# Kernel optimization log

Measured on AMD Instinct MI355X. Metric: run time of the kernel, lower is better.

## Reference

```python
import jax, jax.numpy as jnp
import numpy as np

B, T, V, D = 8, 256, 32, 256


def setup_inputs() -> dict:
    key = jax.random.key(0)
    k1, k2 = jax.random.split(key)
    # scale by 0.1 so exp(q.k) stays well within fp32 range (dot std ~ 0.1^2*sqrt(D))
    feature = jax.random.normal(k1, (B, T, V, D), dtype=jnp.float32) * 0.1
    feature_aug = jax.random.normal(k2, (B, T, V, D), dtype=jnp.float32) * 0.1
    return {"feature": feature, "feature_aug": feature_aug}


def reference(feature, feature_aug):
    # match torch permute(0,2,1,3): [B,T,V,D] -> [B,V,T,D]
    f = jnp.transpose(feature, (0, 2, 1, 3))      # [B,V,Tq,D]
    fa = jnp.transpose(feature_aug, (0, 2, 1, 3))  # [B,V,Tk,D]
    # all-pairs QK^T scores: [B_i, B_j, V, Tq, Tk]
    scores = jnp.einsum('ivqd,jvkd->ijvqk', f, fa)
    E = jnp.exp(scores)
    # positive (j == i): ap = exp(scores[i,i]).sum over V, Tq -> [B, Tk]
    diag = jnp.einsum('iivqk->ivqk', E)           # [B,V,Tq,Tk]
    ap_exp = diag.sum(axis=(1, 2))                # [B, Tk]
    # negatives (j != i): sum over j,V,Tk minus the j==i part -> [B, Tq]
    total = E.sum(axis=(1, 2, 4))                 # [B, Tq]
    self_part = diag.sum(axis=(1, 3))             # [B, Tq]
    an_exp = total - self_part                    # [B, Tq]
    # per-anchor loss vector [T]; original sums over anchors then takes .mean()
    loss_vec = -jnp.log(ap_exp / an_exp)          # [B, T]
    return loss_vec.sum(axis=0).mean()
```

## Files before the change

kernel.cpp:

```cpp
#include <hip/hip_runtime.h>
#include <hip/hip_bf16.h>


typedef __attribute__((ext_vector_type(4))) float f32x4;
typedef __attribute__((ext_vector_type(4))) int   i32x4;
typedef __attribute__((ext_vector_type(8))) int   i32x8;
typedef __attribute__((ext_vector_type(8))) __bf16 bf16x8;

#if __has_builtin(__builtin_amdgcn_exp2f)
#define EXP2(x) __builtin_amdgcn_exp2f(x)
#else
#define EXP2(x) exp2f(x)
#endif

__device__ __forceinline__ unsigned short f2bf(float f) {
    unsigned u = __builtin_bit_cast(unsigned, f);
    u += 0x7FFFu + ((u >> 16) & 1u);
    return (unsigned short)(u >> 16);
}

template <bool HI>
__device__ __forceinline__ unsigned cvt2fp8(float a, float b, unsigned old) {
    return __builtin_amdgcn_cvt_pk_fp8_f32(a, b, old, HI);
}
__device__ __forceinline__ unsigned pack4fp8(float x, float y, float z, float w) {
    return cvt2fp8<true>(z, w, cvt2fp8<false>(x, y, 0u));
}

__device__ __forceinline__ void async16(const void* g, void* l) {
    __builtin_amdgcn_global_load_lds(
        (const __attribute__((address_space(1))) unsigned int*)g,
        (__attribute__((address_space(3))) unsigned int*)l,
        16, 0, 0);
}

__device__ __forceinline__ i32x8 cat8(i32x4 lo, i32x4 hi) {
    i32x8 r;
    r[0] = lo[0]; r[1] = lo[1]; r[2] = lo[2]; r[3] = lo[3];
    r[4] = hi[0]; r[5] = hi[1]; r[6] = hi[2]; r[7] = hi[3];
    return r;
}

template <int CTRL>
__device__ __forceinline__ float dpp_add(float x) {
    int y = __builtin_amdgcn_update_dpp(0, __builtin_bit_cast(int, x),
                                        CTRL, 0xf, 0xf, true);
    return x + __builtin_bit_cast(float, y);
}
__device__ __forceinline__ float rowsum16(float x) {
    x = dpp_add<0x111>(x);
    x = dpp_add<0x112>(x);
    x = dpp_add<0x114>(x);
    x = dpp_add<0x118>(x);
    return x;
}

__global__ __launch_bounds__(256) void infonce_repack_fp8(
    const float* __restrict__ feat, const float* __restrict__ feat_aug,
    unsigned char* __restrict__ pA, unsigned char* __restrict__ pB,
    float* __restrict__ counters)
{
    const int row = blockIdx.x;
    const int tid = threadIdx.x;
    if (blockIdx.x == 0 && blockIdx.y == 0) {
        #pragma unroll
        for (int k = 0; k < 24; ++k) counters[k * 256 + tid] = 0.f;
    }
    const bool isA = (blockIdx.y == 0);
    const float sc = isA ? 1.4426950408889634f : 1.0f;
    const float* src = (isA ? feat : feat_aug) + (size_t)row * 8192;
    unsigned char* dst = (isA ? pA : pB) + (size_t)row * 8192;
    #pragma unroll
    for (int it = 0; it < 2; ++it) {
        const int base = it * 4096 + tid * 16;
        const float4 f0 = *(const float4*)(src + base);
        const float4 f1 = *(const float4*)(src + base + 4);
        const float4 f2 = *(const float4*)(src + base + 8);
        const float4 f3 = *(const float4*)(src + base + 12);
        uint4 p;
        p.x = pack4fp8(f0.x*sc, f0.y*sc, f0.z*sc, f0.w*sc);
        p.y = pack4fp8(f1.x*sc, f1.y*sc, f1.z*sc, f1.w*sc);
        p.z = pack4fp8(f2.x*sc, f2.y*sc, f2.z*sc, f2.w*sc);
        p.w = pack4fp8(f3.x*sc, f3.y*sc, f3.z*sc, f3.w*sc);
        *(uint4*)(dst + base) = p;
    }
}

__global__ __launch_bounds__(256, 2) void infonce_main_nl(
    const unsigned char* __restrict__ pA, const unsigned char* __restrict__ pB,
    float* __restrict__ total, float* __restrict__ selfp, float* __restrict__ ap)
{
    __shared__ __align__(16) unsigned char As[128 * 256];
    __shared__ __align__(16) unsigned char Bs[2][64 * 256];
    float (*ls_row2)[128]  = (float (*)[128])(void*)As;
    float (*ls_self2)[128] = (float (*)[128])(void*)(As + 1024);

    const int tid  = threadIdx.x;
    const int lane = tid & 63;
    const int w    = tid >> 6;
    const int wm   = w >> 1;
    const int wn   = w & 1;
    const int lrow = lane & 15;
    const int quad = lane >> 4;

    const int tileM = blockIdx.x;
    const int v     = blockIdx.y;
    const int nD0   = (tileM >> 1) * 4;

    const size_t vOff = (size_t)v * 256;

    {
        const size_t rowM = (size_t)(tileM * 128 + w * 32 + quad) * 8192 + vOff;
        #pragma unroll
        for (int i = 0; i < 8; ++i) {
            const int lg = (lrow ^ ((i * 4 + quad) & 15)) << 4;
            async16(pA + rowM + (size_t)i * 4 * 8192 + lg, &As[(w * 32 + i * 4) * 256]);
        }
    }
    const size_t rowNbase = (size_t)(w * 16 + quad) * 8192 + vOff;
    #pragma unroll
    for (int i = 0; i < 4; ++i) {
        const int lg = (lrow ^ ((i * 4 + quad) & 15)) << 4;
        async16(pB + rowNbase + (size_t)i * 4 * 8192 + lg,
                &Bs[0][(w * 16 + i * 4) * 256]);
    }
    __syncthreads();

    i32x8 af[2][4];
    #pragma unroll
    for (int h = 0; h < 2; ++h)
        #pragma unroll
        for (int t = 0; t < 4; ++t) {
            const int rA = (wm * 64 + t * 16 + lrow) * 256;
            const int g0 = ((h * 8 + quad * 2) ^ lrow) * 16;
            af[h][t] = cat8(*(const i32x4*)&As[rA + g0],
                            *(const i32x4*)&As[rA + (g0 ^ 16)]);
        }

    float rowp[4][4];
    float selfr[4][4];
    #pragma unroll
    for (int t = 0; t < 4; ++t)
        #pragma unroll
        for (int r = 0; r < 4; ++r) { rowp[t][r] = 0.f; selfr[t][r] = 0.f; }

    for (int n = 0; n < 32; ++n) {
        const int b = n & 1;
        if (n < 31) {
            const unsigned char* src = pB + rowNbase + (size_t)(n + 1) * 64 * 8192;
            #pragma unroll
            for (int i = 0; i < 4; ++i) {
                const int lg = (lrow ^ ((i * 4 + quad) & 15)) << 4;
                async16(src + (size_t)i * 4 * 8192 + lg,
                        &Bs[b ^ 1][(w * 16 + i * 4) * 256]);
            }
        }
        f32x4 acc[4][2];
        #pragma unroll
        for (int t = 0; t < 4; ++t)
            #pragma unroll
            for (int tj = 0; tj < 2; ++tj)
                acc[t][tj] = (f32x4){0.f, 0.f, 0.f, 0.f};
        #pragma unroll
        for (int h = 0; h < 2; ++h) {
            i32x8 bf[2];
            #pragma unroll
            for (int tj = 0; tj < 2; ++tj) {
                const int rB = (wn * 32 + tj * 16 + lrow) * 256;
                const int g0 = ((h * 8 + quad * 2) ^ lrow) * 16;
                bf[tj] = cat8(*(const i32x4*)&Bs[b][rB + g0],
                              *(const i32x4*)&Bs[b][rB + (g0 ^ 16)]);
            }
            #pragma unroll
            for (int ti = 0; ti < 4; ++ti)
                #pragma unroll
                for (int tj = 0; tj < 2; ++tj)
                    acc[ti][tj] = __builtin_amdgcn_mfma_scale_f32_16x16x128_f8f6f4(
                        af[h][ti], bf[tj], acc[ti][tj],
                        0, 0, 0, 127, 0, 127);
        }
        const bool diagIter = (n >= nD0) && (n < nD0 + 4);
        float colp0 = 0.f, colp1 = 0.f;
        #pragma unroll
        for (int t = 0; t < 4; ++t)
            #pragma unroll
            for (int r = 0; r < 4; ++r) {
                float e0 = EXP2(acc[t][0][r]);
                float e1 = EXP2(acc[t][1][r]);
                rowp[t][r] += e0 + e1;
                if (diagIter) { selfr[t][r] += e0 + e1; colp0 += e0; colp1 += e1; }
            }
        if (diagIter) {
            float q0 = colp0, q1 = colp1;
            q0 += __shfl_xor(q0, 16); q0 += __shfl_xor(q0, 32);
            q1 += __shfl_xor(q1, 16); q1 += __shfl_xor(q1, 32);
            if (lane < 16) {
                atomicAdd(&ap[n * 64 + wn * 32 + lane], q0);
                atomicAdd(&ap[n * 64 + wn * 32 + 16 + lane], q1);
            }
        }
        __syncthreads();
    }

    #pragma unroll
    for (int t = 0; t < 4; ++t)
        #pragma unroll
        for (int r = 0; r < 4; ++r) {
            float rs = rowsum16(rowp[t][r]);
            float ss = rowsum16(selfr[t][r]);
            if (lrow == 15) {
                const int idx = wm * 64 + t * 16 + quad * 4 + r;
                ls_row2[wn][idx]  = rs;
                ls_self2[wn][idx] = ss;
            }
        }
    __syncthreads();
    if (tid < 128) {
        atomicAdd(&total[tileM * 128 + tid], ls_row2[0][tid] + ls_row2[1][tid]);
    } else {
        const int t2 = tid - 128;
        atomicAdd(&selfp[tileM * 128 + t2], ls_self2[0][t2] + ls_self2[1][t2]);
    }
}

__global__ __launch_bounds__(256) void infonce_main_slow(
    const float* __restrict__ feat, const float* __restrict__ feat_aug,
    float* __restrict__ total, float* __restrict__ selfp, float* __restrict__ ap)
{
    __shared__ __align__(16) unsigned short As[128][72];
    __shared__ __align__(16) unsigned short Bs[128][72];
    __shared__ float ls_row[128];
    __shared__ float ls_col[128];

    const int tid  = threadIdx.x;
    const int lane = tid & 63;
    const int w    = tid >> 6;
    const int wm   = w >> 1;
    const int wn   = w & 1;
    const int lrow = lane & 15;
    const int quad = lane >> 4;

    const int tileM = blockIdx.x & 15;
    const int tileN = blockIdx.x >> 4;
    const int v     = blockIdx.y;
    const bool diag = (tileM >> 1) == (tileN >> 1);

    if (tid < 128) ls_row[tid] = 0.0f;
    else           ls_col[tid - 128] = 0.0f;

    const float* aBase = feat     + (size_t)v * 256;
    const float* bBase = feat_aug + (size_t)v * 256;

    f32x4 acc[4][4];
    #pragma unroll
    for (int i = 0; i < 4; ++i)
        #pragma unroll
        for (int j = 0; j < 4; ++j)
            acc[i][j] = (f32x4){0.f, 0.f, 0.f, 0.f};

    const int srow = tid >> 4;
    const int scol = (tid & 15) * 4;

    for (int s = 0; s < 4; ++s) {
        const int k0 = s * 64;
        if (s) __syncthreads();
        #pragma unroll
        for (int it = 0; it < 8; ++it) {
            const int row = it * 16 + srow;
            const float4 a4 = *(const float4*)(aBase + (size_t)(tileM * 128 + row) * 8192 + k0 + scol);
            const float4 b4 = *(const float4*)(bBase + (size_t)(tileN * 128 + row) * 8192 + k0 + scol);
            uint2 wa, wb;
            wa.x = (unsigned)f2bf(a4.x) | ((unsigned)f2bf(a4.y) << 16);
            wa.y = (unsigned)f2bf(a4.z) | ((unsigned)f2bf(a4.w) << 16);
            wb.x = (unsigned)f2bf(b4.x) | ((unsigned)f2bf(b4.y) << 16);
            wb.y = (unsigned)f2bf(b4.z) | ((unsigned)f2bf(b4.w) << 16);
            *(uint2*)&As[row][scol] = wa;
            *(uint2*)&Bs[row][scol] = wb;
        }
        __syncthreads();
        #pragma unroll
        for (int kk = 0; kk < 64; kk += 32) {
            bf16x8 af[4], bfr[4];
            #pragma unroll
            for (int t = 0; t < 4; ++t) {
                af[t]  = *(const bf16x8*)&As[wm * 64 + t * 16 + lrow][kk + quad * 8];
                bfr[t] = *(const bf16x8*)&Bs[wn * 64 + t * 16 + lrow][kk + quad * 8];
            }
            #pragma unroll
            for (int ti = 0; ti < 4; ++ti)
                #pragma unroll
                for (int tj = 0; tj < 4; ++tj)
                    acc[ti][tj] = __builtin_amdgcn_mfma_f32_16x16x32_bf16(
                        af[ti], bfr[tj], acc[ti][tj], 0, 0, 0);
        }
    }

    float colp[4] = {0.f, 0.f, 0.f, 0.f};
    #pragma unroll
    for (int ti = 0; ti < 4; ++ti) {
        #pragma unroll
        for (int r = 0; r < 4; ++r) {
            float e0 = __expf(acc[ti][0][r]);
            float e1 = __expf(acc[ti][1][r]);
            float e2 = __expf(acc[ti][2][r]);
            float e3 = __expf(acc[ti][3][r]);
            colp[0] += e0; colp[1] += e1; colp[2] += e2; colp[3] += e3;
            float rp = (e0 + e1) + (e2 + e3);
            rp += __shfl_xor(rp, 1);
            rp += __shfl_xor(rp, 2);
            rp += __shfl_xor(rp, 4);
            rp += __shfl_xor(rp, 8);
            if (lrow == 0)
                atomicAdd(&ls_row[wm * 64 + ti * 16 + quad * 4 + r], rp);
        }
    }
    if (diag) {
        #pragma unroll
        for (int tj = 0; tj < 4; ++tj) {
            float q = colp[tj];
            q += __shfl_xor(q, 16);
            q += __shfl_xor(q, 32);
            if (lane < 16)
                atomicAdd(&ls_col[wn * 64 + tj * 16 + lane], q);
        }
    }
    __syncthreads();
    if (tid < 128) {
        const float rs = ls_row[tid];
        const int rowg = tileM * 128 + tid;
        atomicAdd(&total[rowg], rs);
        if (diag) atomicAdd(&selfp[rowg], rs);
    } else if (diag) {
        const int t2 = tid - 128;
        atomicAdd(&ap[tileN * 128 + t2], ls_col[t2]);
    }
}

__global__ __launch_bounds__(256) void infonce_finalize(
    const float* __restrict__ total, const float* __restrict__ selfp,
    const float* __restrict__ ap, float* __restrict__ out)
{
    __shared__ float red[4];
    const int tid = threadIdx.x;
    float s = 0.f;
    for (int e = tid; e < 2048; e += 256) {
        const float an = total[e] - selfp[e];
        s += logf(an / ap[e]);
    }
    #pragma unroll
    for (int m = 32; m >= 1; m >>= 1) s += __shfl_xor(s, m);
    if ((tid & 63) == 0) red[tid >> 6] = s;
    __syncthreads();
    if (tid == 0) out[0] = (red[0] + red[1] + red[2] + red[3]) * (1.0f / 256.0f);
}

extern "C" void kernel_launch(void* const* d_in, const int* in_sizes, int n_in,
                              void* d_out, int out_size, void* d_ws, size_t ws_size,
                              hipStream_t stream) {
    const float* feat     = (const float*)d_in[0];
    const float* feat_aug = (const float*)d_in[1];
    float* total = (float*)d_ws;
    float* selfp = total + 2048;
    float* ap    = selfp + 2048;

    const size_t packBytes = (size_t)2048 * 8192;
    const size_t need = 32768 + 2 * packBytes;
    if (ws_size >= need) {
        unsigned char* pA = (unsigned char*)d_ws + 32768;
        unsigned char* pB = pA + packBytes;
        infonce_repack_fp8<<<dim3(2048, 2), 256, 0, stream>>>(feat, feat_aug, pA, pB, total);
        infonce_main_nl<<<dim3(16, 32), 256, 0, stream>>>(pA, pB, total, selfp, ap);
    } else {
        (void)hipMemsetAsync(d_ws, 0, 3 * 2048 * sizeof(float), stream);
        infonce_main_slow<<<dim3(256, 32), 256, 0, stream>>>(feat, feat_aug, total, selfp, ap);
    }
    infonce_finalize<<<1, 256, 0, stream>>>(total, selfp, ap, (float*)d_out);
}
```

Before: 192.8 us.

## Fuse A-side fp8 packing into main kernel and split N loop across two blocks

Drops the separate fp8 repack of the query features. The main kernel now loads fp32 rows directly into registers and converts them to fp8 with the log2e scale applied, which removes a global write and re-read of the packed A buffer and frees the A shared-memory tile. The N loop over key tiles is split across a new grid z dimension of 2 so there are twice as many blocks, and the occupancy hint is raised to 3. In exchange, each half re-reads the fp32 A rows, and there are more atomic adds into the row totals, with the self term added only by the block that covers the diagonal.

```diff
diff --git a/kernel.cpp b/kernel.cpp
--- a/kernel.cpp
+++ b/kernel.cpp
@@ -12,6 +12,8 @@
 #else
 #define EXP2(x) exp2f(x)
 #endif
+
+#define LOG2E 1.4426950408889634f
 
 __device__ __forceinline__ unsigned short f2bf(float f) {
     unsigned u = __builtin_bit_cast(unsigned, f);
@@ -56,20 +58,17 @@
 }
 
 __global__ __launch_bounds__(256) void infonce_repack_fp8(
-    const float* __restrict__ feat, const float* __restrict__ feat_aug,
-    unsigned char* __restrict__ pA, unsigned char* __restrict__ pB,
+    const float* __restrict__ feat_aug, unsigned char* __restrict__ pB,
     float* __restrict__ counters)
 {
     const int row = blockIdx.x;
     const int tid = threadIdx.x;
-    if (blockIdx.x == 0 && blockIdx.y == 0) {
+    if (row == 0) {
         #pragma unroll
         for (int k = 0; k < 24; ++k) counters[k * 256 + tid] = 0.f;
     }
-    const bool isA = (blockIdx.y == 0);
-    const float sc = isA ? 1.4426950408889634f : 1.0f;
-    const float* src = (isA ? feat : feat_aug) + (size_t)row * 8192;
-    unsigned char* dst = (isA ? pA : pB) + (size_t)row * 8192;
+    const float* src = feat_aug + (size_t)row * 8192;
+    unsigned char* dst = pB + (size_t)row * 8192;
     #pragma unroll
     for (int it = 0; it < 2; ++it) {
         const int base = it * 4096 + tid * 16;
@@ -78,22 +77,21 @@
         const float4 f2 = *(const float4*)(src + base + 8);
         const float4 f3 = *(const float4*)(src + base + 12);
         uint4 p;
-        p.x = pack4fp8(f0.x*sc, f0.y*sc, f0.z*sc, f0.w*sc);
-        p.y = pack4fp8(f1.x*sc, f1.y*sc, f1.z*sc, f1.w*sc);
-        p.z = pack4fp8(f2.x*sc, f2.y*sc, f2.z*sc, f2.w*sc);
-        p.w = pack4fp8(f3.x*sc, f3.y*sc, f3.z*sc, f3.w*sc);
+        p.x = pack4fp8(f0.x, f0.y, f0.z, f0.w);
+        p.y = pack4fp8(f1.x, f1.y, f1.z, f1.w);
+        p.z = pack4fp8(f2.x, f2.y, f2.z, f2.w);
+        p.w = pack4fp8(f3.x, f3.y, f3.z, f3.w);
         *(uint4*)(dst + base) = p;
     }
 }
 
-__global__ __launch_bounds__(256, 2) void infonce_main_nl(
-    const unsigned char* __restrict__ pA, const unsigned char* __restrict__ pB,
+__global__ __launch_bounds__(256, 3) void infonce_main_nl(
+    const float* __restrict__ feat, const unsigned char* __restrict__ pB,
     float* __restrict__ total, float* __restrict__ selfp, float* __restrict__ ap)
 {
-    __shared__ __align__(16) unsigned char As[128 * 256];
     __shared__ __align__(16) unsigned char Bs[2][64 * 256];
-    float (*ls_row2)[128]  = (float (*)[128])(void*)As;
-    float (*ls_self2)[128] = (float (*)[128])(void*)(As + 1024);
+    float (*ls_row2)[128]  = (float (*)[128])(void*)&Bs[0][0];
+    float (*ls_self2)[128] = (float (*)[128])(void*)&Bs[0][1024];
 
     const int tid  = threadIdx.x;
     const int lane = tid & 63;
@@ -105,37 +103,43 @@
 
     const int tileM = blockIdx.x;
     const int v     = blockIdx.y;
+    const int zh    = blockIdx.z;
+    const int n0    = zh * 16;
+    const int n1    = n0 + 16;
     const int nD0   = (tileM >> 1) * 4;
+    const bool hasDiag = (nD0 >= n0) && (nD0 < n1);
 
     const size_t vOff = (size_t)v * 256;
 
+    const size_t rowNbase = (size_t)(w * 16 + quad) * 8192 + vOff;
     {
-        const size_t rowM = (size_t)(tileM * 128 + w * 32 + quad) * 8192 + vOff;
-        #pragma unroll
-        for (int i = 0; i < 8; ++i) {
+        const unsigned char* srcB = pB + rowNbase + (size_t)n0 * 64 * 8192;
+        #pragma unroll
+        for (int i = 0; i < 4; ++i) {
             const int lg = (lrow ^ ((i * 4 + quad) & 15)) << 4;
-            async16(pA + rowM + (size_t)i * 4 * 8192 + lg, &As[(w * 32 + i * 4) * 256]);
-        }
-    }
-    const size_t rowNbase = (size_t)(w * 16 + quad) * 8192 + vOff;
-    #pragma unroll
-    for (int i = 0; i < 4; ++i) {
-        const int lg = (lrow ^ ((i * 4 + quad) & 15)) << 4;
-        async16(pB + rowNbase + (size_t)i * 4 * 8192 + lg,
-                &Bs[0][(w * 16 + i * 4) * 256]);
-    }
-    __syncthreads();
+            async16(srcB + (size_t)i * 4 * 8192 + lg,
+                    &Bs[0][(w * 16 + i * 4) * 256]);
+        }
+    }
 
     i32x8 af[2][4];
     #pragma unroll
-    for (int h = 0; h < 2; ++h)
-        #pragma unroll
-        for (int t = 0; t < 4; ++t) {
-            const int rA = (wm * 64 + t * 16 + lrow) * 256;
-            const int g0 = ((h * 8 + quad * 2) ^ lrow) * 16;
-            af[h][t] = cat8(*(const i32x4*)&As[rA + g0],
-                            *(const i32x4*)&As[rA + (g0 ^ 16)]);
-        }
+    for (int t = 0; t < 4; ++t) {
+        const float* rowA = feat +
+            (size_t)(tileM * 128 + wm * 64 + t * 16 + lrow) * 8192 + vOff;
+        #pragma unroll
+        for (int h = 0; h < 2; ++h) {
+            const float* s = rowA + h * 128 + quad * 32;
+            i32x8 r;
+            #pragma unroll
+            for (int m = 0; m < 8; ++m) {
+                const float4 f = *(const float4*)(s + m * 4);
+                r[m] = pack4fp8(f.x * LOG2E, f.y * LOG2E,
+                                f.z * LOG2E, f.w * LOG2E);
+            }
+            af[h][t] = r;
+        }
+    }
 
     float rowp[4][4];
     float selfr[4][4];
@@ -144,9 +148,11 @@
         #pragma unroll
         for (int r = 0; r < 4; ++r) { rowp[t][r] = 0.f; selfr[t][r] = 0.f; }
 
-    for (int n = 0; n < 32; ++n) {
-        const int b = n & 1;
-        if (n < 31) {
+    __syncthreads();
+
+    for (int n = n0; n < n1; ++n) {
+        const int b = (n - n0) & 1;
+        if (n < n1 - 1) {
             const unsigned char* src = pB + rowNbase + (size_t)(n + 1) * 64 * 8192;
             #pragma unroll
             for (int i = 0; i < 4; ++i) {
@@ -217,7 +223,7 @@
     __syncthreads();
     if (tid < 128) {
         atomicAdd(&total[tileM * 128 + tid], ls_row2[0][tid] + ls_row2[1][tid]);
-    } else {
+    } else if (hasDiag) {
         const int t2 = tid - 128;
         atomicAdd(&selfp[tileM * 128 + t2], ls_self2[0][t2] + ls_self2[1][t2]);
     }
@@ -364,12 +370,11 @@
     float* ap    = selfp + 2048;
 
     const size_t packBytes = (size_t)2048 * 8192;
-    const size_t need = 32768 + 2 * packBytes;
+    const size_t need = 32768 + packBytes;
     if (ws_size >= need) {
-        unsigned char* pA = (unsigned char*)d_ws + 32768;
-        unsigned char* pB = pA + packBytes;
-        infonce_repack_fp8<<<dim3(2048, 2), 256, 0, stream>>>(feat, feat_aug, pA, pB, total);
-        infonce_main_nl<<<dim3(16, 32), 256, 0, stream>>>(pA, pB, total, selfp, ap);
+        unsigned char* pB = (unsigned char*)d_ws + 32768;
+        infonce_repack_fp8<<<dim3(2048), 256, 0, stream>>>(feat_aug, pB, total);
+        infonce_main_nl<<<dim3(16, 32, 2), 256, 0, stream>>>(feat, pB, total, selfp, ap);
     } else {
         (void)hipMemsetAsync(d_ws, 0, 3 * 2048 * sizeof(float), stream);
         infonce_main_slow<<<dim3(256, 32), 256, 0, stream>>>(feat, feat_aug, total, selfp, ap);
```

Measured after the change: 232.8 us. 20.8% more time.

## Split N loop across grid z, load A fragments directly from global, raise occupancy

Applied to the files above, without the earlier changes.

Launches twice as many blocks by splitting the 32 B-column tiles into two halves over blockIdx.z, with partial row sums combined through the existing atomics. The A-tile LDS staging is removed: each lane loads its fp8 A fragments straight from global into registers. The reduction scratch now aliases the B buffer. Together these free shared memory and allow a launch bound of 4 blocks per CU, aiming to fix the underfilled 512-block grid on the many-CU device. In exchange, A is read twice from global, atomic traffic on totals doubles, and register pressure may rise under the tighter launch bound.

```diff
diff --git a/kernel.cpp b/kernel.cpp
--- a/kernel.cpp
+++ b/kernel.cpp
@@ -86,14 +86,13 @@
     }
 }
 
-__global__ __launch_bounds__(256, 2) void infonce_main_nl(
+__global__ __launch_bounds__(256, 4) void infonce_main_nl(
     const unsigned char* __restrict__ pA, const unsigned char* __restrict__ pB,
     float* __restrict__ total, float* __restrict__ selfp, float* __restrict__ ap)
 {
-    __shared__ __align__(16) unsigned char As[128 * 256];
     __shared__ __align__(16) unsigned char Bs[2][64 * 256];
-    float (*ls_row2)[128]  = (float (*)[128])(void*)As;
-    float (*ls_self2)[128] = (float (*)[128])(void*)(As + 1024);
+    float (*ls_row2)[128]  = (float (*)[128])(void*)&Bs[0][0];
+    float (*ls_self2)[128] = (float (*)[128])(void*)&Bs[0][1024];
 
     const int tid  = threadIdx.x;
     const int lane = tid & 63;
@@ -105,37 +104,36 @@
 
     const int tileM = blockIdx.x;
     const int v     = blockIdx.y;
+    const int zh    = blockIdx.z;
+    const int n0    = zh * 16;
+    const int n1    = n0 + 16;
     const int nD0   = (tileM >> 1) * 4;
+    const bool hasDiag = (nD0 >= n0) && (nD0 < n1);
 
     const size_t vOff = (size_t)v * 256;
 
+    const size_t rowNbase = (size_t)(w * 16 + quad) * 8192 + vOff;
     {
-        const size_t rowM = (size_t)(tileM * 128 + w * 32 + quad) * 8192 + vOff;
-        #pragma unroll
-        for (int i = 0; i < 8; ++i) {
+        const unsigned char* srcB = pB + rowNbase + (size_t)n0 * 64 * 8192;
+        #pragma unroll
+        for (int i = 0; i < 4; ++i) {
             const int lg = (lrow ^ ((i * 4 + quad) & 15)) << 4;
-            async16(pA + rowM + (size_t)i * 4 * 8192 + lg, &As[(w * 32 + i * 4) * 256]);
-        }
-    }
-    const size_t rowNbase = (size_t)(w * 16 + quad) * 8192 + vOff;
-    #pragma unroll
-    for (int i = 0; i < 4; ++i) {
-        const int lg = (lrow ^ ((i * 4 + quad) & 15)) << 4;
-        async16(pB + rowNbase + (size_t)i * 4 * 8192 + lg,
-                &Bs[0][(w * 16 + i * 4) * 256]);
-    }
-    __syncthreads();
+            async16(srcB + (size_t)i * 4 * 8192 + lg,
+                    &Bs[0][(w * 16 + i * 4) * 256]);
+        }
+    }
 
     i32x8 af[2][4];
     #pragma unroll
-    for (int h = 0; h < 2; ++h)
-        #pragma unroll
-        for (int t = 0; t < 4; ++t) {
-            const int rA = (wm * 64 + t * 16 + lrow) * 256;
-            const int g0 = ((h * 8 + quad * 2) ^ lrow) * 16;
-            af[h][t] = cat8(*(const i32x4*)&As[rA + g0],
-                            *(const i32x4*)&As[rA + (g0 ^ 16)]);
-        }
+    for (int t = 0; t < 4; ++t) {
+        const unsigned char* rowA = pA +
+            (size_t)(tileM * 128 + wm * 64 + t * 16 + lrow) * 8192 + vOff;
+        #pragma unroll
+        for (int h = 0; h < 2; ++h) {
+            const unsigned char* s = rowA + h * 128 + quad * 32;
+            af[h][t] = cat8(*(const i32x4*)s, *(const i32x4*)(s + 16));
+        }
+    }
 
     float rowp[4][4];
     float selfr[4][4];
@@ -144,9 +142,11 @@
         #pragma unroll
         for (int r = 0; r < 4; ++r) { rowp[t][r] = 0.f; selfr[t][r] = 0.f; }
 
-    for (int n = 0; n < 32; ++n) {
-        const int b = n & 1;
-        if (n < 31) {
+    __syncthreads();
+
+    for (int n = n0; n < n1; ++n) {
+        const int b = (n - n0) & 1;
+        if (n < n1 - 1) {
             const unsigned char* src = pB + rowNbase + (size_t)(n + 1) * 64 * 8192;
             #pragma unroll
             for (int i = 0; i < 4; ++i) {
@@ -217,7 +217,7 @@
     __syncthreads();
     if (tid < 128) {
         atomicAdd(&total[tileM * 128 + tid], ls_row2[0][tid] + ls_row2[1][tid]);
-    } else {
+    } else if (hasDiag) {
         const int t2 = tid - 128;
         atomicAdd(&selfp[tileM * 128 + t2], ls_self2[0][t2] + ls_self2[1][t2]);
     }
@@ -369,7 +369,7 @@
         unsigned char* pA = (unsigned char*)d_ws + 32768;
         unsigned char* pB = pA + packBytes;
         infonce_repack_fp8<<<dim3(2048, 2), 256, 0, stream>>>(feat, feat_aug, pA, pB, total);
-        infonce_main_nl<<<dim3(16, 32), 256, 0, stream>>>(pA, pB, total, selfp, ap);
+        infonce_main_nl<<<dim3(16, 32, 2), 256, 0, stream>>>(pA, pB, total, selfp, ap);
     } else {
         (void)hipMemsetAsync(d_ws, 0, 3 * 2048 * sizeof(float), stream);
         infonce_main_slow<<<dim3(256, 32), 256, 0, stream>>>(feat, feat_aug, total, selfp, ap);
```

Result: slower. 412.4 us (+113.9%).

## Deepen B-tile prefetch to two tiles ahead with explicit vmcnt waits

Applied to the files above, without the earlier changes.

The first two B tiles are now loaded up front, and each iteration prefetches tile n+2 into the buffer it just finished using. Each wave copies its B fragments into registers, then hits a barrier before the buffer is overwritten. Fine-grained s_waitcnt vmcnt/lgkmcnt plus sched_barrier replace the blanket __syncthreads, and the MFMA block runs under raised wave priority. The aim is to hide global-to-LDS latency behind more compute. The cost is two barriers per iteration and more B fragments held in registers.

```diff
diff --git a/kernel.cpp b/kernel.cpp
--- a/kernel.cpp
+++ b/kernel.cpp
@@ -12,6 +12,22 @@
 #else
 #define EXP2(x) exp2f(x)
 #endif
+
+#define WAIT_VMCNT(N)                                              \
+    do {                                                           \
+        asm volatile("s_waitcnt vmcnt(" #N ")" ::: "memory");      \
+        __builtin_amdgcn_sched_barrier(0);                         \
+    } while (0)
+#define WAIT_LGKM0                                                 \
+    do {                                                           \
+        asm volatile("s_waitcnt lgkmcnt(0)" ::: "memory");         \
+        __builtin_amdgcn_sched_barrier(0);                         \
+    } while (0)
+#define BARRIER()                                                  \
+    do {                                                           \
+        __builtin_amdgcn_s_barrier();                              \
+        __builtin_amdgcn_sched_barrier(0);                         \
+    } while (0)
 
 __device__ __forceinline__ unsigned short f2bf(float f) {
     unsigned u = __builtin_bit_cast(unsigned, f);
@@ -119,12 +135,17 @@
     }
     const size_t rowNbase = (size_t)(w * 16 + quad) * 8192 + vOff;
     #pragma unroll
-    for (int i = 0; i < 4; ++i) {
-        const int lg = (lrow ^ ((i * 4 + quad) & 15)) << 4;
-        async16(pB + rowNbase + (size_t)i * 4 * 8192 + lg,
-                &Bs[0][(w * 16 + i * 4) * 256]);
-    }
-    __syncthreads();
+    for (int nn = 0; nn < 2; ++nn) {
+        const unsigned char* srcB = pB + rowNbase + (size_t)nn * 64 * 8192;
+        #pragma unroll
+        for (int i = 0; i < 4; ++i) {
+            const int lg = (lrow ^ ((i * 4 + quad) & 15)) << 4;
+            async16(srcB + (size_t)i * 4 * 8192 + lg,
+                    &Bs[nn][(w * 16 + i * 4) * 256]);
+        }
+    }
+    WAIT_VMCNT(4);
+    BARRIER();
 
     i32x8 af[2][4];
     #pragma unroll
@@ -144,41 +165,51 @@
         #pragma unroll
         for (int r = 0; r < 4; ++r) { rowp[t][r] = 0.f; selfr[t][r] = 0.f; }
 
-    for (int n = 0; n < 32; ++n) {
+    auto iterBody = [&](const int n) {
         const int b = n & 1;
-        if (n < 31) {
-            const unsigned char* src = pB + rowNbase + (size_t)(n + 1) * 64 * 8192;
+        BARRIER();
+
+        i32x8 bfr[2][2];
+        #pragma unroll
+        for (int h = 0; h < 2; ++h)
+            #pragma unroll
+            for (int tj = 0; tj < 2; ++tj) {
+                const int rB = (wn * 32 + tj * 16 + lrow) * 256;
+                const int g0 = ((h * 8 + quad * 2) ^ lrow) * 16;
+                bfr[h][tj] = cat8(*(const i32x4*)&Bs[b][rB + g0],
+                                  *(const i32x4*)&Bs[b][rB + (g0 ^ 16)]);
+            }
+        WAIT_LGKM0;
+        BARRIER();
+
+        if (n < 30) {
+            const unsigned char* src = pB + rowNbase + (size_t)(n + 2) * 64 * 8192;
             #pragma unroll
             for (int i = 0; i < 4; ++i) {
                 const int lg = (lrow ^ ((i * 4 + quad) & 15)) << 4;
                 async16(src + (size_t)i * 4 * 8192 + lg,
-                        &Bs[b ^ 1][(w * 16 + i * 4) * 256]);
-            }
-        }
+                        &Bs[b][(w * 16 + i * 4) * 256]);
+            }
+        }
+
         f32x4 acc[4][2];
         #pragma unroll
         for (int t = 0; t < 4; ++t)
             #pragma unroll
             for (int tj = 0; tj < 2; ++tj)
                 acc[t][tj] = (f32x4){0.f, 0.f, 0.f, 0.f};
-        #pragma unroll
-        for (int h = 0; h < 2; ++h) {
-            i32x8 bf[2];
-            #pragma unroll
-            for (int tj = 0; tj < 2; ++tj) {
-                const int rB = (wn * 32 + tj * 16 + lrow) * 256;
-                const int g0 = ((h * 8 + quad * 2) ^ lrow) * 16;
-                bf[tj] = cat8(*(const i32x4*)&Bs[b][rB + g0],
-                              *(const i32x4*)&Bs[b][rB + (g0 ^ 16)]);
-            }
+        __builtin_amdgcn_s_setprio(1);
+        #pragma unroll
+        for (int h = 0; h < 2; ++h)
             #pragma unroll
             for (int ti = 0; ti < 4; ++ti)
                 #pragma unroll
                 for (int tj = 0; tj < 2; ++tj)
                     acc[ti][tj] = __builtin_amdgcn_mfma_scale_f32_16x16x128_f8f6f4(
-                        af[h][ti], bf[tj], acc[ti][tj],
+                        af[h][ti], bfr[h][tj], acc[ti][tj],
                         0, 0, 0, 127, 0, 127);
-        }
+        __builtin_amdgcn_s_setprio(0);
+
         const bool diagIter = (n >= nD0) && (n < nD0 + 4);
         float colp0 = 0.f, colp1 = 0.f;
         #pragma unroll
@@ -199,8 +230,14 @@
                 atomicAdd(&ap[n * 64 + wn * 32 + 16 + lane], q1);
             }
         }
-        __syncthreads();
-    }
+    };
+
+    for (int n = 0; n < 31; ++n) {
+        WAIT_VMCNT(4);
+        iterBody(n);
+    }
+    WAIT_VMCNT(0);
+    iterBody(31);
 
     #pragma unroll
     for (int t = 0; t < 4; ++t)
```

New measurement: 185.3 us. 1.04x faster.
